# Performance work log

Hardware: AMD Instinct MI355X
Metric: run time of the kernel (lower is better)

## Reference

```python
import jax, jax.numpy as jnp
import numpy as np

# Dims: B=4096 batch, E=8 experts, D=1024 in, H=4096 hidden, O=1024 out.
# Faithful to MoE.forward in training mode: every expert runs on every sample,
# then outputs are combined weighted by softmax gating probabilities.

def setup_inputs() -> dict:
    key = jax.random.key(0)
    ks = jax.random.split(key, 5)
    B, E, D, H, O = 4096, 8, 1024, 4096, 1024
    x = jax.random.normal(ks[0], (B, D), dtype=jnp.float32)
    W1 = jax.random.normal(ks[1], (E, D, H), dtype=jnp.float32) * (1.0 / np.sqrt(D))
    b1 = jnp.zeros((E, H), dtype=jnp.float32)
    W2 = jax.random.normal(ks[2], (E, H, O), dtype=jnp.float32) * (1.0 / np.sqrt(H))
    b2 = jnp.zeros((E, O), dtype=jnp.float32)
    Wg = jax.random.normal(ks[3], (D, E), dtype=jnp.float32) * (1.0 / np.sqrt(D))
    bg = jnp.zeros((E,), dtype=jnp.float32)
    return {"x": x, "W1": W1, "b1": b1, "W2": W2, "b2": b2, "Wg": Wg, "bg": bg}


def reference(x, W1, b1, W2, b2, Wg, bg):
    # gating_net(x.view(B, -1)) -> softmax probabilities [B, E]
    gating_probs = jax.nn.softmax(x @ Wg + bg, axis=-1)
    # expert_outputs = stack([student(x) for student in students], dim=1) -> [B, E, O]
    h = jax.nn.relu(jnp.einsum('bd,edh->beh', x, W1) + b1)  # [B, E, H]
    expert_outputs = jnp.einsum('beh,eho->beo', h, W2) + b2  # [B, E, O]
    # weighted combine: (expert_outputs * probs[..., None]).sum(dim=1)
    outputs = jnp.einsum('beo,be->bo', expert_outputs, gating_probs)  # [B, O]
    return outputs
```

## Files before the change

kernel.cpp:

```cpp
#include <hip/hip_runtime.h>
#include <hip/hip_bf16.h>


#define B_DIM 4096
#define E_DIM 8
#define D_DIM 1024
#define H_DIM 4096
#define O_DIM 1024
#define KTOT  (E_DIM * H_DIM)
#define KSPLIT 4

typedef __attribute__((ext_vector_type(8))) short bf16x8;
typedef __attribute__((ext_vector_type(4))) float f32x4;

__device__ __forceinline__ unsigned short f2bf(float f) {
  union { float f; unsigned u; } c; c.f = f;
  unsigned r = c.u + 0x7fffu + ((c.u >> 16) & 1u);
  return (unsigned short)(r >> 16);
}

__device__ __forceinline__ void gload_lds16(const void* g, void* l) {
  __builtin_amdgcn_global_load_lds(
      (const __attribute__((address_space(1))) void*)g,
      (__attribute__((address_space(3))) void*)l, 16, 0, 0);
}

__device__ __forceinline__ void barfence() {
  asm volatile("" ::: "memory");
  __builtin_amdgcn_s_barrier();
  asm volatile("" ::: "memory");
}

__device__ __forceinline__ unsigned swzA(unsigned o) {
  return o ^ (((o >> 7) & 7u) << 4);
}

__device__ __forceinline__ void stageHalf(const char* gbase, size_t rowBytes, int kByte,
                                          char* seg, int tid) {
  #pragma unroll
  for (int r = 0; r < 2; ++r) {
    unsigned o = (unsigned)((r * 512 + tid) * 16);
    unsigned q = swzA(o);
    gload_lds16(gbase + (size_t)(q >> 7) * rowBytes + kByte + (q & 127), seg + o);
  }
}

template<bool STAGE, int VMN>
__device__ __forceinline__ void tile4(
    char* smem, int bufOff,
    const char* AbC, const char* BbC, size_t rbA, size_t rbB, int kStage,
    int wm, int wn, int lane, int tid, f32x4 (&acc)[8][4])
{
  bf16x8 aF[4][2], bLo[2][2], bHi[2][2];
  const char* aSeg = smem + bufOff + wm * 16384;
  const char* bSeg = smem + bufOff + (2 + (wn >> 1)) * 16384;

  #pragma unroll
  for (int m = 0; m < 4; ++m)
    #pragma unroll
    for (int kk = 0; kk < 2; ++kk) {
      unsigned o = (unsigned)((m * 16 + (lane & 15)) * 128 + kk * 64 + ((lane >> 4) * 16));
      aF[m][kk] = *(const bf16x8*)(aSeg + swzA(o));
    }
  #pragma unroll
  for (int n = 0; n < 2; ++n)
    #pragma unroll
    for (int kk = 0; kk < 2; ++kk) {
      unsigned o = (unsigned)(((wn & 1) * 64 + n * 16 + (lane & 15)) * 128 + kk * 64 + ((lane >> 4) * 16));
      bLo[n][kk] = *(const bf16x8*)(bSeg + swzA(o));
    }
  asm volatile("s_waitcnt lgkmcnt(8)" ::: "memory");
  barfence();
  asm volatile("s_waitcnt lgkmcnt(0)" ::: "memory");
  __builtin_amdgcn_s_setprio(1);
  #pragma unroll
  for (int m = 0; m < 4; ++m)
    #pragma unroll
    for (int n = 0; n < 2; ++n)
      #pragma unroll
      for (int kk = 0; kk < 2; ++kk)
        acc[m][n] = __builtin_amdgcn_mfma_f32_16x16x32_bf16(aF[m][kk], bLo[n][kk], acc[m][n], 0, 0, 0);
  __builtin_amdgcn_s_setprio(0);
  barfence();

  #pragma unroll
  for (int n = 0; n < 2; ++n)
    #pragma unroll
    for (int kk = 0; kk < 2; ++kk) {
      unsigned o = (unsigned)(((wn & 1) * 64 + (2 + n) * 16 + (lane & 15)) * 128 + kk * 64 + ((lane >> 4) * 16));
      bHi[n][kk] = *(const bf16x8*)(bSeg + swzA(o));
    }
  barfence();
  asm volatile("s_waitcnt lgkmcnt(0)" ::: "memory");
  __builtin_amdgcn_s_setprio(1);
  #pragma unroll
  for (int m = 0; m < 4; ++m)
    #pragma unroll
    for (int n = 0; n < 2; ++n)
      #pragma unroll
      for (int kk = 0; kk < 2; ++kk)
        acc[m][2 + n] = __builtin_amdgcn_mfma_f32_16x16x32_bf16(aF[m][kk], bHi[n][kk], acc[m][2 + n], 0, 0, 0);
  __builtin_amdgcn_s_setprio(0);
  barfence();

  #pragma unroll
  for (int m = 0; m < 4; ++m)
    #pragma unroll
    for (int kk = 0; kk < 2; ++kk) {
      unsigned o = (unsigned)(((4 + m) * 16 + (lane & 15)) * 128 + kk * 64 + ((lane >> 4) * 16));
      aF[m][kk] = *(const bf16x8*)(aSeg + swzA(o));
    }
  if (STAGE) {
    stageHalf(BbC,                     rbB, kStage, smem + bufOff + 2 * 16384, tid);
    stageHalf(BbC + (size_t)128 * rbB, rbB, kStage, smem + bufOff + 3 * 16384, tid);
  }
  barfence();
  asm volatile("s_waitcnt lgkmcnt(0)" ::: "memory");
  __builtin_amdgcn_s_setprio(1);
  #pragma unroll
  for (int m = 0; m < 4; ++m)
    #pragma unroll
    for (int n = 0; n < 2; ++n)
      #pragma unroll
      for (int kk = 0; kk < 2; ++kk)
        acc[4 + m][2 + n] = __builtin_amdgcn_mfma_f32_16x16x32_bf16(aF[m][kk], bHi[n][kk], acc[4 + m][2 + n], 0, 0, 0);
  __builtin_amdgcn_s_setprio(0);
  barfence();

  if (STAGE) {
    stageHalf(AbC,                     rbA, kStage, smem + bufOff + 0,     tid);
    stageHalf(AbC + (size_t)128 * rbA, rbA, kStage, smem + bufOff + 16384, tid);
  }
  if (VMN == 8)      asm volatile("s_waitcnt vmcnt(8)" ::: "memory");
  else if (VMN == 0) asm volatile("s_waitcnt vmcnt(0)" ::: "memory");
  barfence();
  __builtin_amdgcn_s_setprio(1);
  #pragma unroll
  for (int m = 0; m < 4; ++m)
    #pragma unroll
    for (int n = 0; n < 2; ++n)
      #pragma unroll
      for (int kk = 0; kk < 2; ++kk)
        acc[4 + m][n] = __builtin_amdgcn_mfma_f32_16x16x32_bf16(aF[m][kk], bLo[n][kk], acc[4 + m][n], 0, 0, 0);
  __builtin_amdgcn_s_setprio(0);
  barfence();
}

template<int MODE>
__global__ __launch_bounds__(512, 2)
void gemm8p(const unsigned short* __restrict__ A,
            const unsigned short* __restrict__ Bt,
            void* __restrict__ Cout,
            const float* __restrict__ probs,
            const float* __restrict__ bias,
            int M, int N, int K, int kChunk)
{
  __shared__ __align__(16) char smem[131072];

  const int tid = threadIdx.x;
  const int wave = tid >> 6, lane = tid & 63;
  const int wm = wave >> 2, wn = wave & 3;

  int mt, nt, kBeg;
  if (MODE == 1) {
    int bid = blockIdx.x;
    int xcd = bid & 7, seq = bid >> 3;
    int grp = seq >> 4, g = seq & 15;
    mt = (grp & 3) * 4 + (g & 3);
    nt = xcd * 16 + (grp >> 2) * 4 + (g >> 2);
    kBeg = 0;
  } else {
    int x = blockIdx.x;
    mt = (x & 7) * 2 + ((x >> 3) & 1);
    nt = x >> 4;
    kBeg = blockIdx.y * kChunk;
  }

  const char* AbC = (const char*)(A + (size_t)mt * 256 * K);
  const char* BbC = (const char*)(Bt + (size_t)nt * 256 * K);
  const size_t rbA = (size_t)K * 2, rbB = (size_t)K * 2;

  f32x4 acc[8][4] = {};

  const int NT = kChunk / 64;
  const int NI = NT / 2;

  {
    int k0 = kBeg * 2, k1 = (kBeg + 64) * 2;
    stageHalf(BbC,                    rbB, k0, smem + 2 * 16384, tid);
    stageHalf(BbC + (size_t)128 * rbB, rbB, k0, smem + 3 * 16384, tid);
    stageHalf(AbC,                    rbA, k0, smem + 0,         tid);
    stageHalf(AbC + (size_t)128 * rbA, rbA, k0, smem + 16384,    tid);
    stageHalf(BbC,                    rbB, k1, smem + 65536 + 2 * 16384, tid);
    stageHalf(BbC + (size_t)128 * rbB, rbB, k1, smem + 65536 + 3 * 16384, tid);
    stageHalf(AbC,                    rbA, k1, smem + 65536 + 0,         tid);
    stageHalf(AbC + (size_t)128 * rbA, rbA, k1, smem + 65536 + 16384,    tid);
  }
  asm volatile("s_waitcnt vmcnt(8)" ::: "memory");
  barfence();

  for (int i = 0; i < NI - 1; ++i) {
    int ks0 = (kBeg + (2 * i + 2) * 64) * 2;
    int ks1 = (kBeg + (2 * i + 3) * 64) * 2;
    tile4<true, 8>(smem, 0,     AbC, BbC, rbA, rbB, ks0, wm, wn, lane, tid, acc);
    tile4<true, 8>(smem, 65536, AbC, BbC, rbA, rbB, ks1, wm, wn, lane, tid, acc);
  }
  tile4<false, 0>(smem, 0,     AbC, BbC, rbA, rbB, 0, wm, wn, lane, tid, acc);
  tile4<false, -1>(smem, 65536, AbC, BbC, rbA, rbB, 0, wm, wn, lane, tid, acc);

  const int colBase = nt * 256 + wn * 64;
  const int rowBase = mt * 256 + wm * 128;

  if (MODE == 1) {
    char* myseg = smem + wave * 16384;
    const int eIdx = colBase >> 12;
    #pragma unroll
    for (int m = 0; m < 8; ++m) {
      #pragma unroll
      for (int n = 0; n < 4; ++n) {
        const int col = colBase + n * 16 + (lane & 15);
        const float bv = bias[col];
        #pragma unroll
        for (int j = 0; j < 4; ++j) {
          const int row = rowBase + m * 16 + ((lane >> 4) * 4) + j;
          float v = acc[m][n][j] + bv;
          v = fmaxf(v, 0.0f) * probs[row * E_DIM + eIdx];
          *(unsigned short*)(myseg + (m * 16 + ((lane >> 4) * 4) + j) * 128 +
                             (n * 16 + (lane & 15)) * 2) = f2bf(v);
        }
      }
    }
    unsigned short* Cw = (unsigned short*)Cout;
    const int lc = (lane & 7) * 8;
    #pragma unroll
    for (int i = 0; i < 16; ++i) {
      int lr = i * 8 + (lane >> 3);
      bf16x8 vv = *(const bf16x8*)(myseg + lr * 128 + lc * 2);
      *(bf16x8*)(&Cw[(size_t)(rowBase + lr) * N + colBase + lc]) = vv;
    }
  } else {
    float* dst = (float*)Cout + (size_t)blockIdx.y * M * N;
    #pragma unroll
    for (int m = 0; m < 8; ++m) {
      #pragma unroll
      for (int n = 0; n < 4; ++n) {
        const int col = colBase + n * 16 + (lane & 15);
        #pragma unroll
        for (int j = 0; j < 4; ++j) {
          const int row = rowBase + m * 16 + ((lane >> 4) * 4) + j;
          dst[(size_t)row * N + col] = acc[m][n][j];
        }
      }
    }
  }
}

__global__ __launch_bounds__(256) void gating_kernel(
    const float* __restrict__ x, const float* __restrict__ Wg,
    const float* __restrict__ bg, float* __restrict__ probs)
{
  __shared__ float sWg[D_DIM * E_DIM];
  for (int i = threadIdx.x; i < D_DIM * E_DIM; i += 256) sWg[i] = Wg[i];
  __syncthreads();

  const int wave = threadIdx.x >> 6, lane = threadIdx.x & 63;
  const int b = blockIdx.x * 4 + wave;

  float acc[E_DIM] = {};
  const float* xr = x + (size_t)b * D_DIM;
  #pragma unroll
  for (int i = 0; i < D_DIM / 64; ++i) {
    int d = i * 64 + lane;
    float xv = xr[d];
    #pragma unroll
    for (int e = 0; e < E_DIM; ++e) acc[e] += xv * sWg[d * E_DIM + e];
  }
  #pragma unroll
  for (int e = 0; e < E_DIM; ++e) {
    #pragma unroll
    for (int off = 32; off > 0; off >>= 1) acc[e] += __shfl_down(acc[e], off);
  }
  if (lane == 0) {
    float m = -1e30f;
    #pragma unroll
    for (int e = 0; e < E_DIM; ++e) { acc[e] += bg[e]; m = fmaxf(m, acc[e]); }
    float p[E_DIM]; float s = 0.f;
    #pragma unroll
    for (int e = 0; e < E_DIM; ++e) { p[e] = expf(acc[e] - m); s += p[e]; }
    float inv = 1.0f / s;
    #pragma unroll
    for (int e = 0; e < E_DIM; ++e) probs[(size_t)b * E_DIM + e] = p[e] * inv;
  }
}

__global__ __launch_bounds__(256) void convert_x_kernel(
    const float* __restrict__ x, unsigned short* __restrict__ xb)
{
  int i = blockIdx.x * 256 + threadIdx.x;
  const float4* src = (const float4*)x;
  float4 v = src[i];
  union { unsigned short u[4]; unsigned long long q; } o;
  o.u[0] = f2bf(v.x); o.u[1] = f2bf(v.y); o.u[2] = f2bf(v.z); o.u[3] = f2bf(v.w);
  *(unsigned long long*)(xb + (size_t)i * 4) = o.q;
}

__global__ __launch_bounds__(256) void transpose_cvt(
    const float* __restrict__ src, unsigned short* __restrict__ dst,
    int ldSrc, int ldDst, size_t srcPlane, size_t dstPlane)
{
  __shared__ float t[64][65];
  const int e = blockIdx.z;
  const int x0 = blockIdx.x * 64;
  const int y0 = blockIdx.y * 64;
  const float* s = src + (size_t)e * srcPlane;
  unsigned short* d = dst + (size_t)e * dstPlane;

  const int rr = threadIdx.x >> 4;
  const int cc = (threadIdx.x & 15) * 4;
  #pragma unroll
  for (int i = 0; i < 4; ++i) {
    int r = rr + 16 * i;
    float4 v = *(const float4*)&s[(size_t)(x0 + r) * ldSrc + y0 + cc];
    t[r][cc] = v.x; t[r][cc + 1] = v.y; t[r][cc + 2] = v.z; t[r][cc + 3] = v.w;
  }
  __syncthreads();

  const int x4 = (threadIdx.x & 15) * 4;
  const int yb = threadIdx.x >> 4;
  #pragma unroll
  for (int j = 0; j < 4; ++j) {
    int y = yb + 16 * j;
    union { unsigned short u[4]; unsigned long long q; } o;
    #pragma unroll
    for (int q = 0; q < 4; ++q) o.u[q] = f2bf(t[x4 + q][y]);
    *(unsigned long long*)(d + (size_t)(y0 + y) * ldDst + x0 + x4) = o.q;
  }
}

__global__ __launch_bounds__(256) void reduce_out(
    const float* __restrict__ partial, const float* __restrict__ probs,
    const float* __restrict__ b2, float* __restrict__ out)
{
  const int i = blockIdx.x * 256 + threadIdx.x;
  const int row = i >> 8;
  const int colv = i & 255;
  const size_t plane = (size_t)B_DIM * O_DIM / 4;

  float4 v = make_float4(0.f, 0.f, 0.f, 0.f);
  #pragma unroll
  for (int ks = 0; ks < KSPLIT; ++ks) {
    float4 p = ((const float4*)partial)[ks * plane + i];
    v.x += p.x; v.y += p.y; v.z += p.z; v.w += p.w;
  }
  #pragma unroll
  for (int e = 0; e < E_DIM; ++e) {
    float pe = probs[row * E_DIM + e];
    float4 b = ((const float4*)b2)[e * (O_DIM / 4) + colv];
    v.x += pe * b.x; v.y += pe * b.y; v.z += pe * b.z; v.w += pe * b.w;
  }
  ((float4*)out)[i] = v;
}

extern "C" void kernel_launch(void* const* d_in, const int* in_sizes, int n_in,
                              void* d_out, int out_size, void* d_ws, size_t ws_size,
                              hipStream_t stream)
{
  const float* x  = (const float*)d_in[0];
  const float* W1 = (const float*)d_in[1];
  const float* b1 = (const float*)d_in[2];
  const float* W2 = (const float*)d_in[3];
  const float* b2 = (const float*)d_in[4];
  const float* Wg = (const float*)d_in[5];
  const float* bg = (const float*)d_in[6];
  float* out = (float*)d_out;

  char* ws = (char*)d_ws;
  float*          probs = (float*)ws;
  unsigned short* xb    = (unsigned short*)(ws + (1u << 17));
  unsigned short* W1t   = (unsigned short*)(ws + (1u << 17) + (8u << 20));
  unsigned short* W2t   = (unsigned short*)(ws + (1u << 17) + (8u << 20) + (64u << 20));
  unsigned short* hp    = (unsigned short*)(ws + (1u << 17) + (8u << 20) + (128u << 20));
  float* partial = (float*)W1t;

  gating_kernel<<<B_DIM / 4, 256, 0, stream>>>(x, Wg, bg, probs);
  convert_x_kernel<<<(B_DIM * D_DIM / 4) / 256, 256, 0, stream>>>(x, xb);
  transpose_cvt<<<dim3(D_DIM / 64, H_DIM / 64, E_DIM), 256, 0, stream>>>(
      W1, W1t, H_DIM, D_DIM, (size_t)D_DIM * H_DIM, (size_t)H_DIM * D_DIM);
  transpose_cvt<<<dim3(H_DIM / 64, O_DIM / 64, E_DIM), 256, 0, stream>>>(
      W2, W2t, O_DIM, KTOT, (size_t)H_DIM * O_DIM, (size_t)H_DIM);

  gemm8p<1><<<dim3((B_DIM / 256) * (KTOT / 256), 1), 512, 0, stream>>>(
      xb, W1t, hp, probs, b1, B_DIM, KTOT, D_DIM, D_DIM);

  gemm8p<2><<<dim3((B_DIM / 256) * (O_DIM / 256), KSPLIT), 512, 0, stream>>>(
      hp, W2t, partial, probs, nullptr, B_DIM, O_DIM, KTOT, KTOT / KSPLIT);

  reduce_out<<<(B_DIM * O_DIM / 4) / 256, 256, 0, stream>>>(partial, probs, b2, out);
}
```

Measured before the change: 962.5 us.

## Precompute swizzled LDS/global addresses and trim barriers in GEMM main loop

Replaces per-iteration swizzle address arithmetic with precomputed per-lane LDS offsets (using XOR 64 for the second k-half) and incrementing global stage pointers. It also removes several barriers and lgkmcnt waits between MFMA phases, so LDS reads can overlap with compute. The epilogue's LDS staging now uses the swizzle to avoid bank conflicts. This cuts scalar/VALU overhead and sync stalls, at the cost of relying on compiler-inserted waits for correctness and looser ordering around buffer reuse.

```diff
diff --git a/kernel.cpp b/kernel.cpp
--- a/kernel.cpp
+++ b/kernel.cpp
@@ -35,115 +35,109 @@
   return o ^ (((o >> 7) & 7u) << 4);
 }
 
-__device__ __forceinline__ void stageHalf(const char* gbase, size_t rowBytes, int kByte,
-                                          char* seg, int tid) {
-  #pragma unroll
-  for (int r = 0; r < 2; ++r) {
-    unsigned o = (unsigned)((r * 512 + tid) * 16);
-    unsigned q = swzA(o);
-    gload_lds16(gbase + (size_t)(q >> 7) * rowBytes + kByte + (q & 127), seg + o);
-  }
+struct StagePtrs { const char *b0a, *b0b, *b1a, *b1b, *a0a, *a0b, *a1a, *a1b; };
+
+__device__ __forceinline__ void stage8(StagePtrs& sp, char* smem, int bufOff, unsigned dstT) {
+  char* d = smem + bufOff + dstT;
+  gload_lds16(sp.b0a, d + 2 * 16384);        sp.b0a += 128;
+  gload_lds16(sp.b0b, d + 2 * 16384 + 8192); sp.b0b += 128;
+  gload_lds16(sp.b1a, d + 3 * 16384);        sp.b1a += 128;
+  gload_lds16(sp.b1b, d + 3 * 16384 + 8192); sp.b1b += 128;
+  gload_lds16(sp.a0a, d + 0);                sp.a0a += 128;
+  gload_lds16(sp.a0b, d + 8192);             sp.a0b += 128;
+  gload_lds16(sp.a1a, d + 16384);            sp.a1a += 128;
+  gload_lds16(sp.a1b, d + 16384 + 8192);     sp.a1b += 128;
 }
 
 template<bool STAGE, int VMN>
-__device__ __forceinline__ void tile4(
-    char* smem, int bufOff,
-    const char* AbC, const char* BbC, size_t rbA, size_t rbB, int kStage,
-    int wm, int wn, int lane, int tid, f32x4 (&acc)[8][4])
-{
-  bf16x8 aF[4][2], bLo[2][2], bHi[2][2];
-  const char* aSeg = smem + bufOff + wm * 16384;
-  const char* bSeg = smem + bufOff + (2 + (wn >> 1)) * 16384;
-
+__device__ __forceinline__ void tileK(
+    char* smem, int bufOff, unsigned aRel, unsigned bRel,
+    StagePtrs& sp, unsigned dstT, f32x4 (&acc)[8][4])
+{
+  const char* pA0 = smem + bufOff + aRel;
+  const char* pA1 = (const char*)((uintptr_t)pA0 ^ 64);
+  const char* pB0 = smem + bufOff + bRel;
+  const char* pB1 = (const char*)((uintptr_t)pB0 ^ 64);
+
+  bf16x8 aL0[4], aL1[4], aH0[4], aH1[4], bL0[2], bL1[2], bH0[2], bH1[2];
+
+  #pragma unroll
+  for (int m = 0; m < 4; ++m) {
+    aL0[m] = *(const bf16x8*)(pA0 + m * 2048);
+    aL1[m] = *(const bf16x8*)(pA1 + m * 2048);
+  }
+  #pragma unroll
+  for (int n = 0; n < 2; ++n) {
+    bL0[n] = *(const bf16x8*)(pB0 + n * 2048);
+    bL1[n] = *(const bf16x8*)(pB1 + n * 2048);
+  }
+  __builtin_amdgcn_s_setprio(1);
   #pragma unroll
   for (int m = 0; m < 4; ++m)
     #pragma unroll
-    for (int kk = 0; kk < 2; ++kk) {
-      unsigned o = (unsigned)((m * 16 + (lane & 15)) * 128 + kk * 64 + ((lane >> 4) * 16));
-      aF[m][kk] = *(const bf16x8*)(aSeg + swzA(o));
-    }
-  #pragma unroll
-  for (int n = 0; n < 2; ++n)
-    #pragma unroll
-    for (int kk = 0; kk < 2; ++kk) {
-      unsigned o = (unsigned)(((wn & 1) * 64 + n * 16 + (lane & 15)) * 128 + kk * 64 + ((lane >> 4) * 16));
-      bLo[n][kk] = *(const bf16x8*)(bSeg + swzA(o));
-    }
-  asm volatile("s_waitcnt lgkmcnt(8)" ::: "memory");
-  barfence();
-  asm volatile("s_waitcnt lgkmcnt(0)" ::: "memory");
+    for (int n = 0; n < 2; ++n) {
+      acc[m][n] = __builtin_amdgcn_mfma_f32_16x16x32_bf16(aL0[m], bL0[n], acc[m][n], 0, 0, 0);
+      acc[m][n] = __builtin_amdgcn_mfma_f32_16x16x32_bf16(aL1[m], bL1[n], acc[m][n], 0, 0, 0);
+    }
+  __builtin_amdgcn_s_setprio(0);
+
+  #pragma unroll
+  for (int n = 0; n < 2; ++n) {
+    bH0[n] = *(const bf16x8*)(pB0 + (2 + n) * 2048);
+    bH1[n] = *(const bf16x8*)(pB1 + (2 + n) * 2048);
+  }
   __builtin_amdgcn_s_setprio(1);
   #pragma unroll
   for (int m = 0; m < 4; ++m)
     #pragma unroll
-    for (int n = 0; n < 2; ++n)
-      #pragma unroll
-      for (int kk = 0; kk < 2; ++kk)
-        acc[m][n] = __builtin_amdgcn_mfma_f32_16x16x32_bf16(aF[m][kk], bLo[n][kk], acc[m][n], 0, 0, 0);
+    for (int n = 0; n < 2; ++n) {
+      acc[m][2 + n] = __builtin_amdgcn_mfma_f32_16x16x32_bf16(aL0[m], bH0[n], acc[m][2 + n], 0, 0, 0);
+      acc[m][2 + n] = __builtin_amdgcn_mfma_f32_16x16x32_bf16(aL1[m], bH1[n], acc[m][2 + n], 0, 0, 0);
+    }
   __builtin_amdgcn_s_setprio(0);
   barfence();
 
   #pragma unroll
-  for (int n = 0; n < 2; ++n)
-    #pragma unroll
-    for (int kk = 0; kk < 2; ++kk) {
-      unsigned o = (unsigned)(((wn & 1) * 64 + (2 + n) * 16 + (lane & 15)) * 128 + kk * 64 + ((lane >> 4) * 16));
-      bHi[n][kk] = *(const bf16x8*)(bSeg + swzA(o));
-    }
-  barfence();
-  asm volatile("s_waitcnt lgkmcnt(0)" ::: "memory");
+  for (int m = 0; m < 4; ++m) {
+    aH0[m] = *(const bf16x8*)(pA0 + (4 + m) * 2048);
+    aH1[m] = *(const bf16x8*)(pA1 + (4 + m) * 2048);
+  }
+  if (STAGE) {
+    char* d = smem + bufOff + dstT;
+    gload_lds16(sp.b0a, d + 2 * 16384);        sp.b0a += 128;
+    gload_lds16(sp.b0b, d + 2 * 16384 + 8192); sp.b0b += 128;
+    gload_lds16(sp.b1a, d + 3 * 16384);        sp.b1a += 128;
+    gload_lds16(sp.b1b, d + 3 * 16384 + 8192); sp.b1b += 128;
+  }
   __builtin_amdgcn_s_setprio(1);
   #pragma unroll
   for (int m = 0; m < 4; ++m)
     #pragma unroll
-    for (int n = 0; n < 2; ++n)
-      #pragma unroll
-      for (int kk = 0; kk < 2; ++kk)
-        acc[m][2 + n] = __builtin_amdgcn_mfma_f32_16x16x32_bf16(aF[m][kk], bHi[n][kk], acc[m][2 + n], 0, 0, 0);
+    for (int n = 0; n < 2; ++n) {
+      acc[4 + m][2 + n] = __builtin_amdgcn_mfma_f32_16x16x32_bf16(aH0[m], bH0[n], acc[4 + m][2 + n], 0, 0, 0);
+      acc[4 + m][2 + n] = __builtin_amdgcn_mfma_f32_16x16x32_bf16(aH1[m], bH1[n], acc[4 + m][2 + n], 0, 0, 0);
+    }
   __builtin_amdgcn_s_setprio(0);
   barfence();
 
+  if (STAGE) {
+    char* d = smem + bufOff + dstT;
+    gload_lds16(sp.a0a, d + 0);                sp.a0a += 128;
+    gload_lds16(sp.a0b, d + 8192);             sp.a0b += 128;
+    gload_lds16(sp.a1a, d + 16384);            sp.a1a += 128;
+    gload_lds16(sp.a1b, d + 16384 + 8192);     sp.a1b += 128;
+  }
+  if (VMN == 8)      { asm volatile("s_waitcnt vmcnt(8)" ::: "memory"); barfence(); }
+  else if (VMN == 0) { asm volatile("s_waitcnt vmcnt(0)" ::: "memory"); barfence(); }
+  __builtin_amdgcn_s_setprio(1);
   #pragma unroll
   for (int m = 0; m < 4; ++m)
     #pragma unroll
-    for (int kk = 0; kk < 2; ++kk) {
-      unsigned o = (unsigned)(((4 + m) * 16 + (lane & 15)) * 128 + kk * 64 + ((lane >> 4) * 16));
-      aF[m][kk] = *(const bf16x8*)(aSeg + swzA(o));
-    }
-  if (STAGE) {
-    stageHalf(BbC,                     rbB, kStage, smem + bufOff + 2 * 16384, tid);
-    stageHalf(BbC + (size_t)128 * rbB, rbB, kStage, smem + bufOff + 3 * 16384, tid);
-  }
-  barfence();
-  asm volatile("s_waitcnt lgkmcnt(0)" ::: "memory");
-  __builtin_amdgcn_s_setprio(1);
-  #pragma unroll
-  for (int m = 0; m < 4; ++m)
-    #pragma unroll
-    for (int n = 0; n < 2; ++n)
-      #pragma unroll
-      for (int kk = 0; kk < 2; ++kk)
-        acc[4 + m][2 + n] = __builtin_amdgcn_mfma_f32_16x16x32_bf16(aF[m][kk], bHi[n][kk], acc[4 + m][2 + n], 0, 0, 0);
+    for (int n = 0; n < 2; ++n) {
+      acc[4 + m][n] = __builtin_amdgcn_mfma_f32_16x16x32_bf16(aH0[m], bL0[n], acc[4 + m][n], 0, 0, 0);
+      acc[4 + m][n] = __builtin_amdgcn_mfma_f32_16x16x32_bf16(aH1[m], bL1[n], acc[4 + m][n], 0, 0, 0);
+    }
   __builtin_amdgcn_s_setprio(0);
-  barfence();
-
-  if (STAGE) {
-    stageHalf(AbC,                     rbA, kStage, smem + bufOff + 0,     tid);
-    stageHalf(AbC + (size_t)128 * rbA, rbA, kStage, smem + bufOff + 16384, tid);
-  }
-  if (VMN == 8)      asm volatile("s_waitcnt vmcnt(8)" ::: "memory");
-  else if (VMN == 0) asm volatile("s_waitcnt vmcnt(0)" ::: "memory");
-  barfence();
-  __builtin_amdgcn_s_setprio(1);
-  #pragma unroll
-  for (int m = 0; m < 4; ++m)
-    #pragma unroll
-    for (int n = 0; n < 2; ++n)
-      #pragma unroll
-      for (int kk = 0; kk < 2; ++kk)
-        acc[4 + m][n] = __builtin_amdgcn_mfma_f32_16x16x32_bf16(aF[m][kk], bLo[n][kk], acc[4 + m][n], 0, 0, 0);
-  __builtin_amdgcn_s_setprio(0);
-  barfence();
 }
 
 template<int MODE>
@@ -155,7 +149,7 @@
             const float* __restrict__ bias,
             int M, int N, int K, int kChunk)
 {
-  __shared__ __align__(16) char smem[131072];
+  __shared__ __align__(128) char smem[131072];
 
   const int tid = threadIdx.x;
   const int wave = tid >> 6, lane = tid & 63;
@@ -178,35 +172,40 @@
 
   const char* AbC = (const char*)(A + (size_t)mt * 256 * K);
   const char* BbC = (const char*)(Bt + (size_t)nt * 256 * K);
-  const size_t rbA = (size_t)K * 2, rbB = (size_t)K * 2;
+  const size_t rb = (size_t)K * 2;
 
   f32x4 acc[8][4] = {};
 
+  const unsigned swzC = (lane & 7u) << 4;
+  const unsigned slotX = (((unsigned)(lane >> 4)) * 16) ^ swzC;
+  const unsigned aRel = (unsigned)(wm * 16384 + (lane & 15) * 128) + slotX;
+  const unsigned bRel = (unsigned)((2 + (wn >> 1)) * 16384 +
+                                   ((wn & 1) * 64 + (lane & 15)) * 128) + slotX;
+  const unsigned dstT = (unsigned)(tid * 16);
+
+  const unsigned Cs = (((unsigned)(tid >> 3)) & 7u) << 4;
+  const unsigned q0 = ((unsigned)(tid * 16)) ^ Cs;
+  StagePtrs sp;
+  {
+    const char* bA = AbC + (size_t)kBeg * 2 + (size_t)(q0 >> 7) * rb + (q0 & 127);
+    const char* bB = BbC + (size_t)kBeg * 2 + (size_t)(q0 >> 7) * rb + (q0 & 127);
+    sp.a0a = bA;            sp.a0b = bA + 64 * rb;
+    sp.a1a = bA + 128 * rb; sp.a1b = bA + 192 * rb;
+    sp.b0a = bB;            sp.b0b = bB + 64 * rb;
+    sp.b1a = bB + 128 * rb; sp.b1b = bB + 192 * rb;
+  }
+
   const int NT = kChunk / 64;
-  const int NI = NT / 2;
-
-  {
-    int k0 = kBeg * 2, k1 = (kBeg + 64) * 2;
-    stageHalf(BbC,                    rbB, k0, smem + 2 * 16384, tid);
-    stageHalf(BbC + (size_t)128 * rbB, rbB, k0, smem + 3 * 16384, tid);
-    stageHalf(AbC,                    rbA, k0, smem + 0,         tid);
-    stageHalf(AbC + (size_t)128 * rbA, rbA, k0, smem + 16384,    tid);
-    stageHalf(BbC,                    rbB, k1, smem + 65536 + 2 * 16384, tid);
-    stageHalf(BbC + (size_t)128 * rbB, rbB, k1, smem + 65536 + 3 * 16384, tid);
-    stageHalf(AbC,                    rbA, k1, smem + 65536 + 0,         tid);
-    stageHalf(AbC + (size_t)128 * rbA, rbA, k1, smem + 65536 + 16384,    tid);
-  }
+
+  stage8(sp, smem, 0, dstT);
+  stage8(sp, smem, 65536, dstT);
   asm volatile("s_waitcnt vmcnt(8)" ::: "memory");
   barfence();
 
-  for (int i = 0; i < NI - 1; ++i) {
-    int ks0 = (kBeg + (2 * i + 2) * 64) * 2;
-    int ks1 = (kBeg + (2 * i + 3) * 64) * 2;
-    tile4<true, 8>(smem, 0,     AbC, BbC, rbA, rbB, ks0, wm, wn, lane, tid, acc);
-    tile4<true, 8>(smem, 65536, AbC, BbC, rbA, rbB, ks1, wm, wn, lane, tid, acc);
-  }
-  tile4<false, 0>(smem, 0,     AbC, BbC, rbA, rbB, 0, wm, wn, lane, tid, acc);
-  tile4<false, -1>(smem, 65536, AbC, BbC, rbA, rbB, 0, wm, wn, lane, tid, acc);
+  for (int t = 0; t < NT - 2; ++t)
+    tileK<true, 8>(smem, (t & 1) * 65536, aRel, bRel, sp, dstT, acc);
+  tileK<false, 0>(smem, ((NT - 2) & 1) * 65536, aRel, bRel, sp, dstT, acc);
+  tileK<false, -1>(smem, ((NT - 1) & 1) * 65536, aRel, bRel, sp, dstT, acc);
 
   const int colBase = nt * 256 + wn * 64;
   const int rowBase = mt * 256 + wm * 128;
@@ -225,8 +224,9 @@
           const int row = rowBase + m * 16 + ((lane >> 4) * 4) + j;
           float v = acc[m][n][j] + bv;
           v = fmaxf(v, 0.0f) * probs[row * E_DIM + eIdx];
-          *(unsigned short*)(myseg + (m * 16 + ((lane >> 4) * 4) + j) * 128 +
-                             (n * 16 + (lane & 15)) * 2) = f2bf(v);
+          unsigned off = (unsigned)((m * 16 + ((lane >> 4) * 4) + j) * 128 +
+                                    (n * 16 + (lane & 15)) * 2);
+          *(unsigned short*)(myseg + swzA(off)) = f2bf(v);
         }
       }
     }
@@ -235,7 +235,7 @@
     #pragma unroll
     for (int i = 0; i < 16; ++i) {
       int lr = i * 8 + (lane >> 3);
-      bf16x8 vv = *(const bf16x8*)(myseg + lr * 128 + lc * 2);
+      bf16x8 vv = *(const bf16x8*)(myseg + swzA((unsigned)(lr * 128 + lc * 2)));
       *(bf16x8*)(&Cw[(size_t)(rowBase + lr) * N + colBase + lc]) = vv;
     }
   } else {
```

New measurement: 1.010 ms. 1.05x slower.
